# Performance work log

Hardware: AMD Instinct MI355X
Metric: run time of the kernel (lower is better)

The kernel has to match this reference:

```python
import jax, jax.numpy as jnp
import numpy as np

B, S, F = 256, 512, 26
H, M, C = 512, 256, 20  # rnn_hidden, mlp_hidden, num_classes


def setup_inputs() -> dict:
    key = jax.random.key(0)
    ks = jax.random.split(key, 9)
    s_ih = 1.0 / np.sqrt(H)
    return {
        "x": jax.random.normal(ks[0], (B, S, F), dtype=jnp.float32),
        "w_ih": jax.random.uniform(ks[1], (4 * H, F), jnp.float32, -s_ih, s_ih),
        "w_hh": jax.random.uniform(ks[2], (4 * H, H), jnp.float32, -s_ih, s_ih),
        "b_ih": jax.random.uniform(ks[3], (4 * H,), jnp.float32, -s_ih, s_ih),
        "b_hh": jax.random.uniform(ks[4], (4 * H,), jnp.float32, -s_ih, s_ih),
        "w1": jax.random.uniform(ks[5], (M, H), jnp.float32, -s_ih, s_ih),
        "b1": jax.random.uniform(ks[6], (M,), jnp.float32, -s_ih, s_ih),
        "w2": jax.random.uniform(ks[7], (C, M), jnp.float32, -1.0 / np.sqrt(M), 1.0 / np.sqrt(M)),
        "b2": jax.random.uniform(ks[8], (C,), jnp.float32, -1.0 / np.sqrt(M), 1.0 / np.sqrt(M)),
    }


def reference(x, w_ih, w_hh, b_ih, b_hh, w1, b1, w2, b2):
    b, s, _ = x.shape
    h0 = jnp.zeros((b, H), x.dtype)
    c0 = jnp.zeros((b, H), x.dtype)
    bias = b_ih + b_hh

    def step(carry, xt):
        h, c = carry
        # original stores hx.data -> state carried into next step is detached
        h = jax.lax.stop_gradient(h)
        c = jax.lax.stop_gradient(c)
        z = xt @ w_ih.T + h @ w_hh.T + bias  # [b, 4H]
        i, f, g, o = jnp.split(z, 4, axis=-1)  # PyTorch gate order i,f,g,o
        c2 = jax.nn.sigmoid(f) * c + jax.nn.sigmoid(i) * jnp.tanh(g)
        h2 = jax.nn.sigmoid(o) * jnp.tanh(c2)
        return (h2, c2), h2

    _, hs = jax.lax.scan(step, (h0, c0), jnp.transpose(x, (1, 0, 2)))  # hs: [s, b, H]
    hs = jnp.transpose(hs, (1, 0, 2))  # [b, s, H]
    hidden = jax.nn.relu(jnp.einsum("bsh,mh->bsm", hs, w1) + b1)
    logits = jnp.einsum("bsm,cm->bsc", hidden, w2) + b2
    return jax.nn.log_softmax(logits, axis=-1)
```

## Files before the change

kernel.cpp:

```cpp
#include <hip/hip_runtime.h>

#define S_LEN 512
#define HID   512
#define FEAT  26
#define NCLS  20
#define DRING 16

typedef short bf16x8 __attribute__((ext_vector_type(8)));
typedef float f32x4  __attribute__((ext_vector_type(4)));

__device__ __forceinline__ unsigned short f2bf(float f) {
    unsigned u = __builtin_bit_cast(unsigned, f);
    unsigned r = (u + 0x7FFFu + ((u >> 16) & 1u)) >> 16;
    return (unsigned short)r;
}
__device__ __forceinline__ float sigm(float x) { return 1.f / (1.f + __expf(-x)); }
__device__ __forceinline__ float tanh_f(float x) {
    float xc = fminf(fmaxf(x, -15.f), 15.f);
    float t = __expf(-2.f * xc);
    return (1.f - t) / (1.f + t);
}

__device__ __forceinline__ void load4_coherent(const unsigned short* p,
                                               uint4& a0, uint4& a1, uint4& a2, uint4& a3) {
    asm volatile(
        "global_load_dwordx4 %0, %4, off sc0 sc1\n\t"
        "global_load_dwordx4 %1, %5, off sc0 sc1\n\t"
        "global_load_dwordx4 %2, %6, off sc0 sc1\n\t"
        "global_load_dwordx4 %3, %7, off sc0 sc1\n\t"
        "s_waitcnt vmcnt(0)"
        : "=&v"(a0), "=&v"(a1), "=&v"(a2), "=&v"(a3)
        : "v"(p), "v"(p + 8), "v"(p + 16), "v"(p + 24)
        : "memory");
}
__device__ __forceinline__ void store_coherent(unsigned short* p, unsigned d) {
    asm volatile(
        "global_store_dword %0, %1, off sc0 sc1\n\t"
        "s_waitcnt vmcnt(0)"
        :: "v"(p), "v"(d) : "memory");
}
__device__ __forceinline__ void store_coherent_x2(unsigned short* p, unsigned long long d) {
    asm volatile(
        "global_store_dwordx2 %0, %1, off sc0 sc1\n\t"
        "s_waitcnt vmcnt(0)"
        :: "v"(p), "v"(d) : "memory");
}
__device__ __forceinline__ void store_u32_nowait(unsigned* p, unsigned d) {
    asm volatile("global_store_dword %0, %1, off sc0 sc1" :: "v"(p), "v"(d) : "memory");
}
__device__ __forceinline__ unsigned load_u32_coherent(const unsigned* p) {
    unsigned v;
    asm volatile("global_load_dword %0, %1, off sc0 sc1\n\ts_waitcnt vmcnt(0)"
                 : "=v"(v) : "v"(p) : "memory");
    return v;
}

__global__ void prep_kernel(const float* __restrict__ w1, const float* __restrict__ w2,
                            unsigned short* __restrict__ w1b, unsigned short* __restrict__ w2b,
                            unsigned* __restrict__ syncw, int nclear) {
    int i = blockIdx.x * 256 + threadIdx.x;
    if (i < nclear) syncw[i] = 0u;
    if (i < 256 * 512) w1b[i] = f2bf(w1[i]);
    if (i < NCLS * 256) w2b[i] = f2bf(w2[i]);
}

__global__ __launch_bounds__(256, 1) void lstm_big_kernel(
    const float* __restrict__ x,
    const float* __restrict__ w_ih,
    const float* __restrict__ w_hh,
    const float* __restrict__ b_ih,
    const float* __restrict__ b_hh,
    const unsigned short* __restrict__ w1b,
    const float* __restrict__ b1,
    const unsigned short* __restrict__ w2b,
    const float* __restrict__ b2,
    float* __restrict__ out,
    unsigned short* __restrict__ hs,
    unsigned* __restrict__ flags)
{
    const int tid  = threadIdx.x;
    const int wave = tid >> 6;
    const int lane = tid & 63;
    const int quad = lane >> 4;
    const int l16  = lane & 15;
    const int wg   = blockIdx.x;

    __shared__ __align__(16) unsigned short At[16 * 552];
    __shared__ float zb[16 * 260];
    __shared__ __align__(16) unsigned short hid[16 * 264];
    __shared__ float lg[16 * 24];
    __shared__ unsigned rdy;
    if (tid == 0) rdy = 0u;
    __syncthreads();

    if (wg < 128) {
        const int clust = wg >> 3;
        const int wic   = wg & 7;
        const int B0    = clust * 16;
        const int U0    = wic * 64;

        bf16x8 bB[4][17];
#pragma unroll
        for (int tl = 0; tl < 4; ++tl) {
            const int row = wave * 512 + U0 + tl * 16 + l16;
            const float* wrow = w_hh + (size_t)row * HID;
#pragma unroll
            for (int kk = 0; kk < 16; ++kk) {
                const float* p = wrow + kk * 32 + quad * 8;
                bf16x8 v;
#pragma unroll
                for (int j = 0; j < 8; ++j) v[j] = (short)f2bf(p[j]);
                bB[tl][kk] = v;
            }
            const float* irow = w_ih + (size_t)row * FEAT;
            bf16x8 v;
#pragma unroll
            for (int j = 0; j < 8; ++j) {
                int ftr = quad * 8 + j;
                v[j] = (ftr < FEAT) ? (short)f2bf(irow[ftr]) : (short)0;
            }
            bB[tl][16] = v;
        }

        const int gb = tid >> 4;
        const int gu = tid & 15;
        float bias[4][4];
#pragma unroll
        for (int uu = 0; uu < 4; ++uu)
#pragma unroll
            for (int g = 0; g < 4; ++g) {
                int r = g * 512 + U0 + 4 * gu + uu;
                bias[uu][g] = b_ih[r] + b_hh[r];
            }
        float cst[4] = {0.f, 0.f, 0.f, 0.f};

        const int sm = tid >> 4;
        const int sc = tid & 15;
        unsigned short* hsc = hs + (size_t)clust * S_LEN * 16 * HID;
        unsigned* myflag = flags + (clust * 8 + wic) * 16;
        const unsigned* peer = flags + (clust * 8 + (lane & 7)) * 16;

        for (int t = 0; t < S_LEN; ++t) {
            {
                unsigned pk = 0u;
                if (sc <= 12) {
                    float2 xv = *(const float2*)(x + ((size_t)(B0 + sm) * S_LEN + t) * FEAT + sc * 2);
                    pk = (unsigned)f2bf(xv.x) | ((unsigned)f2bf(xv.y) << 16);
                }
                *(unsigned*)(At + sm * 552 + 512 + sc * 2) = pk;
            }
            if (t > 0) {
                if (wave == 0) {
                    for (;;) {
                        unsigned v = load_u32_coherent(peer);
                        if (__ballot(v >= (unsigned)t) == ~0ull) break;
                        __builtin_amdgcn_s_sleep(1);
                    }
                    if (lane == 0)
                        __hip_atomic_store(&rdy, (unsigned)t, __ATOMIC_RELAXED,
                                           __HIP_MEMORY_SCOPE_WORKGROUP);
                } else {
                    while (__hip_atomic_load(&rdy, __ATOMIC_RELAXED,
                                             __HIP_MEMORY_SCOPE_WORKGROUP) < (unsigned)t)
                        __builtin_amdgcn_s_sleep(1);
                }
                const unsigned short* src =
                    hsc + ((size_t)(t - 1) * 16 + sm) * HID + sc * 32;
                unsigned short* dst = At + sm * 552 + sc * 32;
                uint4 a0, a1, a2, a3;
                load4_coherent(src, a0, a1, a2, a3);
                *(uint4*)(dst)      = a0;
                *(uint4*)(dst + 8)  = a1;
                *(uint4*)(dst + 16) = a2;
                *(uint4*)(dst + 24) = a3;
            }
            __syncthreads();

            f32x4 acc[4];
#pragma unroll
            for (int tl = 0; tl < 4; ++tl) acc[tl] = (f32x4){0.f, 0.f, 0.f, 0.f};
            const unsigned short* arow = At + l16 * 552 + quad * 8;
            if (t > 0) {
#pragma unroll
                for (int kk = 0; kk < 17; ++kk) {
                    bf16x8 a = __builtin_bit_cast(bf16x8, *(const uint4*)(arow + kk * 32));
#pragma unroll
                    for (int tl = 0; tl < 4; ++tl)
                        acc[tl] = __builtin_amdgcn_mfma_f32_16x16x32_bf16(a, bB[tl][kk], acc[tl], 0, 0, 0);
                }
            } else {
                bf16x8 a = __builtin_bit_cast(bf16x8, *(const uint4*)(arow + 16 * 32));
#pragma unroll
                for (int tl = 0; tl < 4; ++tl)
                    acc[tl] = __builtin_amdgcn_mfma_f32_16x16x32_bf16(a, bB[tl][16], acc[tl], 0, 0, 0);
            }
#pragma unroll
            for (int tl = 0; tl < 4; ++tl)
#pragma unroll
                for (int r = 0; r < 4; ++r)
                    zb[(quad * 4 + r) * 260 + wave * 64 + tl * 16 + l16] = acc[tl][r];
            __syncthreads();

            {
                const float* zrow = zb + gb * 260;
                unsigned short hv[4];
#pragma unroll
                for (int uu = 0; uu < 4; ++uu) {
                    int u = 4 * gu + uu;
                    float zi = zrow[u]       + bias[uu][0];
                    float zf = zrow[64 + u]  + bias[uu][1];
                    float zg = zrow[128 + u] + bias[uu][2];
                    float zo = zrow[192 + u] + bias[uu][3];
                    float cn = sigm(zf) * cst[uu] + sigm(zi) * tanh_f(zg);
                    cst[uu] = cn;
                    hv[uu] = f2bf(sigm(zo) * tanh_f(cn));
                }
                unsigned long long d = (unsigned long long)hv[0]
                                     | ((unsigned long long)hv[1] << 16)
                                     | ((unsigned long long)hv[2] << 32)
                                     | ((unsigned long long)hv[3] << 48);
                unsigned short* hp = hsc + ((size_t)t * 16 + gb) * HID + U0 + 4 * gu;
                store_coherent_x2(hp, d);
            }
            __syncthreads();
            if (tid == 0) store_u32_nowait(myflag, (unsigned)(t + 1));
        }
    } else {
        const int mwg  = wg - 128;
        const int mc   = mwg >> 3;
        const int m    = mwg & 7;
        const int B0   = mc * 16;
        const unsigned* peer = flags + (mc * 8 + (lane & 7)) * 16;
        const unsigned short* hsc = hs + (size_t)mc * S_LEN * 16 * HID;
        const int sm = tid >> 4;
        const int sc = tid & 15;

        for (int t = m; t < S_LEN; t += 8) {
            if (wave == 0) {
                for (;;) {
                    unsigned v = load_u32_coherent(peer);
                    if (__ballot(v >= (unsigned)(t + 1)) == ~0ull) break;
                    __builtin_amdgcn_s_sleep(8);
                }
                if (lane == 0)
                    __hip_atomic_store(&rdy, (unsigned)(t + 1), __ATOMIC_RELAXED,
                                       __HIP_MEMORY_SCOPE_WORKGROUP);
            } else {
                while (__hip_atomic_load(&rdy, __ATOMIC_RELAXED,
                                         __HIP_MEMORY_SCOPE_WORKGROUP) < (unsigned)(t + 1))
                    __builtin_amdgcn_s_sleep(8);
            }
            {
                const unsigned short* src = hsc + ((size_t)t * 16 + sm) * HID + sc * 32;
                unsigned short* dst = At + sm * 552 + sc * 32;
                uint4 a0, a1, a2, a3;
                load4_coherent(src, a0, a1, a2, a3);
                *(uint4*)(dst)      = a0;
                *(uint4*)(dst + 8)  = a1;
                *(uint4*)(dst + 16) = a2;
                *(uint4*)(dst + 24) = a3;
            }
            __syncthreads();

            f32x4 a1[4];
#pragma unroll
            for (int nt = 0; nt < 4; ++nt) a1[nt] = (f32x4){0.f, 0.f, 0.f, 0.f};
#pragma unroll
            for (int kk = 0; kk < 16; ++kk) {
                bf16x8 a = __builtin_bit_cast(
                    bf16x8, *(const uint4*)(At + l16 * 552 + kk * 32 + quad * 8));
#pragma unroll
                for (int nt = 0; nt < 4; ++nt) {
                    int n = wave * 64 + nt * 16 + l16;
                    bf16x8 b = __builtin_bit_cast(
                        bf16x8, *(const uint4*)(w1b + (size_t)n * 512 + kk * 32 + quad * 8));
                    a1[nt] = __builtin_amdgcn_mfma_f32_16x16x32_bf16(a, b, a1[nt], 0, 0, 0);
                }
            }
#pragma unroll
            for (int nt = 0; nt < 4; ++nt) {
                int n = wave * 64 + nt * 16 + l16;
                float bv = b1[n];
#pragma unroll
                for (int r = 0; r < 4; ++r)
                    hid[(quad * 4 + r) * 264 + n] = f2bf(fmaxf(a1[nt][r] + bv, 0.f));
            }
            __syncthreads();
            if (wave == 0) {
                f32x4 a2[2];
                a2[0] = (f32x4){0.f, 0.f, 0.f, 0.f};
                a2[1] = (f32x4){0.f, 0.f, 0.f, 0.f};
#pragma unroll
                for (int kk = 0; kk < 8; ++kk) {
                    bf16x8 a = __builtin_bit_cast(
                        bf16x8, *(const uint4*)(hid + l16 * 264 + kk * 32 + quad * 8));
#pragma unroll
                    for (int nt = 0; nt < 2; ++nt) {
                        int n = nt * 16 + l16;
                        bf16x8 b;
                        if (n < NCLS) {
                            b = __builtin_bit_cast(
                                bf16x8, *(const uint4*)(w2b + (size_t)n * 256 + kk * 32 + quad * 8));
                        } else {
                            uint4 z; z.x = z.y = z.z = z.w = 0u;
                            b = __builtin_bit_cast(bf16x8, z);
                        }
                        a2[nt] = __builtin_amdgcn_mfma_f32_16x16x32_bf16(a, b, a2[nt], 0, 0, 0);
                    }
                }
#pragma unroll
                for (int nt = 0; nt < 2; ++nt) {
                    int n = nt * 16 + l16;
                    if (n < NCLS) {
                        float bv = b2[n];
#pragma unroll
                        for (int r = 0; r < 4; ++r)
                            lg[(quad * 4 + r) * 24 + n] = a2[nt][r] + bv;
                    }
                }
            }
            __syncthreads();
            if (tid < 16) {
                float v[NCLS];
                float mx = -3.4e38f;
#pragma unroll
                for (int c = 0; c < NCLS; ++c) { v[c] = lg[tid * 24 + c]; mx = fmaxf(mx, v[c]); }
                float s = 0.f;
#pragma unroll
                for (int c = 0; c < NCLS; ++c) s += __expf(v[c] - mx);
                float lse = mx + __logf(s);
                float* orow = out + ((size_t)(B0 + tid) * S_LEN + t) * NCLS;
#pragma unroll
                for (int c = 0; c < NCLS; ++c) orow[c] = v[c] - lse;
            }
            __syncthreads();
        }
    }
}

__global__ __launch_bounds__(256, 2) void lstm_fused_kernel(
    const float* __restrict__ x, const float* __restrict__ w_ih,
    const float* __restrict__ w_hh, const float* __restrict__ b_ih,
    const float* __restrict__ b_hh, const unsigned short* __restrict__ w1b,
    const float* __restrict__ b1, const unsigned short* __restrict__ w2b,
    const float* __restrict__ b2, float* __restrict__ out,
    unsigned short* __restrict__ hb, unsigned* __restrict__ flags,
    unsigned* __restrict__ done)
{
    const int tid  = threadIdx.x;
    const int wave = tid >> 6;
    const int lane = tid & 63;
    const int quad = lane >> 4;
    const int l16  = lane & 15;
    const int wg   = blockIdx.x;

    __shared__ __align__(16) unsigned short At[16 * 552];
    __shared__ float zb[16 * 132];
    __shared__ __align__(16) unsigned short hid[16 * 264];
    __shared__ float lg[16 * 24];
    __shared__ unsigned rdy;
    if (tid == 0) rdy = 0u;
    __syncthreads();

    if (wg < 256) {
        const int clust = (wg & 7) * 2 + (wg >= 128 ? 1 : 0);
        const int wic   = (wg >> 3) & 15;
        const int B0    = clust * 16;
        const int U0    = wic * 32;

        bf16x8 bB[2][17];
#pragma unroll
        for (int tl = 0; tl < 2; ++tl) {
            const int row = wave * 512 + U0 + tl * 16 + l16;
            const float* wrow = w_hh + (size_t)row * HID;
#pragma unroll
            for (int kk = 0; kk < 16; ++kk) {
                const float* p = wrow + kk * 32 + quad * 8;
                bf16x8 v;
#pragma unroll
                for (int j = 0; j < 8; ++j) v[j] = (short)f2bf(p[j]);
                bB[tl][kk] = v;
            }
            const float* irow = w_ih + (size_t)row * FEAT;
            bf16x8 v;
#pragma unroll
            for (int j = 0; j < 8; ++j) {
                int ftr = quad * 8 + j;
                v[j] = (ftr < FEAT) ? (short)f2bf(irow[ftr]) : (short)0;
            }
            bB[tl][16] = v;
        }

        const int gb = tid >> 4;
        const int gu = tid & 15;
        float bias[2][4];
#pragma unroll
        for (int uu = 0; uu < 2; ++uu)
#pragma unroll
            for (int g = 0; g < 4; ++g) {
                int r = g * 512 + U0 + 2 * gu + uu;
                bias[uu][g] = b_ih[r] + b_hh[r];
            }
        float cst[2] = {0.f, 0.f};

        const int sm = tid >> 4;
        const int sc = tid & 15;
        unsigned short* hbc = hb + (size_t)clust * DRING * 16 * HID;
        unsigned* myflag = flags + (clust * 16 + wic) * 16;
        const unsigned* peer = flags + (clust * 16 + (lane & 15)) * 16;

        for (int t = 0; t < S_LEN; ++t) {
            {
                unsigned pk = 0u;
                if (sc <= 12) {
                    float2 xv = *(const float2*)(x + ((size_t)(B0 + sm) * S_LEN + t) * FEAT + sc * 2);
                    pk = (unsigned)f2bf(xv.x) | ((unsigned)f2bf(xv.y) << 16);
                }
                *(unsigned*)(At + sm * 552 + 512 + sc * 2) = pk;
            }
            if (t > 0) {
                if (wave == 0) {
                    if (t >= DRING && lane == 0) {
                        const unsigned* dn = done + (clust * 8 + (t & 7)) * 16;
                        while (load_u32_coherent(dn) < (unsigned)(t - (DRING - 1)))
                            __builtin_amdgcn_s_sleep(8);
                    }
                    for (;;) {
                        unsigned v = load_u32_coherent(peer);
                        if (__ballot(v >= (unsigned)t) == ~0ull) break;
                        __builtin_amdgcn_s_sleep(1);
                    }
                    if (lane == 0)
                        __hip_atomic_store(&rdy, (unsigned)t, __ATOMIC_RELAXED,
                                           __HIP_MEMORY_SCOPE_WORKGROUP);
                } else {
                    while (__hip_atomic_load(&rdy, __ATOMIC_RELAXED,
                                             __HIP_MEMORY_SCOPE_WORKGROUP) < (unsigned)t)
                        __builtin_amdgcn_s_sleep(1);
                }
                const unsigned short* src =
                    hbc + ((t - 1) & (DRING - 1)) * 16 * HID + sm * HID + sc * 32;
                unsigned short* dst = At + sm * 552 + sc * 32;
                uint4 a0, a1, a2, a3;
                load4_coherent(src, a0, a1, a2, a3);
                *(uint4*)(dst)      = a0;
                *(uint4*)(dst + 8)  = a1;
                *(uint4*)(dst + 16) = a2;
                *(uint4*)(dst + 24) = a3;
            }
            __syncthreads();

            f32x4 acc0 = {0.f, 0.f, 0.f, 0.f};
            f32x4 acc1 = {0.f, 0.f, 0.f, 0.f};
            const unsigned short* arow = At + l16 * 552 + quad * 8;
            if (t > 0) {
#pragma unroll
                for (int kk = 0; kk < 17; ++kk) {
                    bf16x8 a = __builtin_bit_cast(bf16x8, *(const uint4*)(arow + kk * 32));
                    acc0 = __builtin_amdgcn_mfma_f32_16x16x32_bf16(a, bB[0][kk], acc0, 0, 0, 0);
                    acc1 = __builtin_amdgcn_mfma_f32_16x16x32_bf16(a, bB[1][kk], acc1, 0, 0, 0);
                }
            } else {
                bf16x8 a = __builtin_bit_cast(bf16x8, *(const uint4*)(arow + 16 * 32));
                acc0 = __builtin_amdgcn_mfma_f32_16x16x32_bf16(a, bB[0][16], acc0, 0, 0, 0);
                acc1 = __builtin_amdgcn_mfma_f32_16x16x32_bf16(a, bB[1][16], acc1, 0, 0, 0);
            }
#pragma unroll
            for (int r = 0; r < 4; ++r) {
                zb[(quad * 4 + r) * 132 + wave * 32 + l16]      = acc0[r];
                zb[(quad * 4 + r) * 132 + wave * 32 + 16 + l16] = acc1[r];
            }
            __syncthreads();

            {
                const float* zrow = zb + gb * 132;
                unsigned short hv2[2];
#pragma unroll
                for (int uu = 0; uu < 2; ++uu) {
                    int u = 2 * gu + uu;
                    float zi = zrow[u]      + bias[uu][0];
                    float zf = zrow[32 + u] + bias[uu][1];
                    float zg = zrow[64 + u] + bias[uu][2];
                    float zo = zrow[96 + u] + bias[uu][3];
                    float cn = sigm(zf) * cst[uu] + sigm(zi) * tanh_f(zg);
                    cst[uu] = cn;
                    hv2[uu] = f2bf(sigm(zo) * tanh_f(cn));
                }
                unsigned short* hp =
                    hbc + (t & (DRING - 1)) * 16 * HID + gb * HID + U0 + 2 * gu;
                store_coherent(hp, (unsigned)hv2[0] | ((unsigned)hv2[1] << 16));
            }
            __syncthreads();
            if (tid == 0) store_u32_nowait(myflag, (unsigned)(t + 1));
        }
    } else {
        const int mwg  = wg - 256;
        const int mc   = mwg >> 3;
        const int m    = mwg & 7;
        const int B0   = mc * 16;
        unsigned* mydone = done + (mc * 8 + m) * 16;
        const unsigned* peer = flags + (mc * 16 + (lane & 15)) * 16;
        const unsigned short* hbc = hb + (size_t)mc * DRING * 16 * HID;
        const int sm = tid >> 4;
        const int sc = tid & 15;

        for (int t = m; t < S_LEN; t += 8) {
            if (wave == 0) {
                for (;;) {
                    unsigned v = load_u32_coherent(peer);
                    if (__ballot(v >= (unsigned)(t + 1)) == ~0ull) break;
                    __builtin_amdgcn_s_sleep(8);
                }
                if (lane == 0)
                    __hip_atomic_store(&rdy, (unsigned)(t + 1), __ATOMIC_RELAXED,
                                       __HIP_MEMORY_SCOPE_WORKGROUP);
            } else {
                while (__hip_atomic_load(&rdy, __ATOMIC_RELAXED,
                                         __HIP_MEMORY_SCOPE_WORKGROUP) < (unsigned)(t + 1))
                    __builtin_amdgcn_s_sleep(8);
            }
            {
                const unsigned short* src =
                    hbc + (t & (DRING - 1)) * 16 * HID + sm * HID + sc * 32;
                unsigned short* dst = At + sm * 552 + sc * 32;
                uint4 a0, a1, a2, a3;
                load4_coherent(src, a0, a1, a2, a3);
                *(uint4*)(dst)      = a0;
                *(uint4*)(dst + 8)  = a1;
                *(uint4*)(dst + 16) = a2;
                *(uint4*)(dst + 24) = a3;
            }
            __syncthreads();
            if (tid == 0) store_u32_nowait(mydone, (unsigned)(t + 1));

            f32x4 a1[4];
#pragma unroll
            for (int nt = 0; nt < 4; ++nt) a1[nt] = (f32x4){0.f, 0.f, 0.f, 0.f};
#pragma unroll
            for (int kk = 0; kk < 16; ++kk) {
                bf16x8 a = __builtin_bit_cast(
                    bf16x8, *(const uint4*)(At + l16 * 552 + kk * 32 + quad * 8));
#pragma unroll
                for (int nt = 0; nt < 4; ++nt) {
                    int n = wave * 64 + nt * 16 + l16;
                    bf16x8 b = __builtin_bit_cast(
                        bf16x8, *(const uint4*)(w1b + (size_t)n * 512 + kk * 32 + quad * 8));
                    a1[nt] = __builtin_amdgcn_mfma_f32_16x16x32_bf16(a, b, a1[nt], 0, 0, 0);
                }
            }
#pragma unroll
            for (int nt = 0; nt < 4; ++nt) {
                int n = wave * 64 + nt * 16 + l16;
                float bv = b1[n];
#pragma unroll
                for (int r = 0; r < 4; ++r)
                    hid[(quad * 4 + r) * 264 + n] = f2bf(fmaxf(a1[nt][r] + bv, 0.f));
            }
            __syncthreads();
            if (wave == 0) {
                f32x4 a2[2];
                a2[0] = (f32x4){0.f, 0.f, 0.f, 0.f};
                a2[1] = (f32x4){0.f, 0.f, 0.f, 0.f};
#pragma unroll
                for (int kk = 0; kk < 8; ++kk) {
                    bf16x8 a = __builtin_bit_cast(
                        bf16x8, *(const uint4*)(hid + l16 * 264 + kk * 32 + quad * 8));
#pragma unroll
                    for (int nt = 0; nt < 2; ++nt) {
                        int n = nt * 16 + l16;
                        bf16x8 b;
                        if (n < NCLS) {
                            b = __builtin_bit_cast(
                                bf16x8, *(const uint4*)(w2b + (size_t)n * 256 + kk * 32 + quad * 8));
                        } else {
                            uint4 z; z.x = z.y = z.z = z.w = 0u;
                            b = __builtin_bit_cast(bf16x8, z);
                        }
                        a2[nt] = __builtin_amdgcn_mfma_f32_16x16x32_bf16(a, b, a2[nt], 0, 0, 0);
                    }
                }
#pragma unroll
                for (int nt = 0; nt < 2; ++nt) {
                    int n = nt * 16 + l16;
                    if (n < NCLS) {
                        float bv = b2[n];
#pragma unroll
                        for (int r = 0; r < 4; ++r)
                            lg[(quad * 4 + r) * 24 + n] = a2[nt][r] + bv;
                    }
                }
            }
            __syncthreads();
            if (tid < 16) {
                float v[NCLS];
                float mx = -3.4e38f;
#pragma unroll
                for (int c = 0; c < NCLS; ++c) { v[c] = lg[tid * 24 + c]; mx = fmaxf(mx, v[c]); }
                float s = 0.f;
#pragma unroll
                for (int c = 0; c < NCLS; ++c) s += __expf(v[c] - mx);
                float lse = mx + __logf(s);
                float* orow = out + ((size_t)(B0 + tid) * S_LEN + t) * NCLS;
#pragma unroll
                for (int c = 0; c < NCLS; ++c) orow[c] = v[c] - lse;
            }
            __syncthreads();
        }
    }
}

extern "C" void kernel_launch(void* const* d_in, const int* in_sizes, int n_in,
                              void* d_out, int out_size, void* d_ws, size_t ws_size,
                              hipStream_t stream) {
    const float* x    = (const float*)d_in[0];
    const float* w_ih = (const float*)d_in[1];
    const float* w_hh = (const float*)d_in[2];
    const float* b_ih = (const float*)d_in[3];
    const float* b_hh = (const float*)d_in[4];
    const float* w1   = (const float*)d_in[5];
    const float* b1   = (const float*)d_in[6];
    const float* w2   = (const float*)d_in[7];
    const float* b2   = (const float*)d_in[8];
    char* ws = (char*)d_ws;

    const size_t HS_BYTES = (size_t)16 * S_LEN * 16 * HID * 2;
    const size_t NEED_BIG = HS_BYTES + 8192 + 262144 + 10240;

    if (ws_size >= NEED_BIG) {
        unsigned short* hsb   = (unsigned short*)ws;
        unsigned*       flags = (unsigned*)(ws + HS_BYTES);
        unsigned short* w1b   = (unsigned short*)(ws + HS_BYTES + 8192);
        unsigned short* w2b   = (unsigned short*)(ws + HS_BYTES + 8192 + 262144);
        prep_kernel<<<512, 256, 0, stream>>>(w1, w2, w1b, w2b, flags, 2048);
        lstm_big_kernel<<<256, 256, 0, stream>>>(x, w_ih, w_hh, b_ih, b_hh,
                                                 w1b, b1, w2b, b2,
                                                 (float*)d_out, hsb, flags);
    } else {
        unsigned short* hb    = (unsigned short*)ws;
        unsigned*       flags = (unsigned*)(ws + 4194304);
        unsigned*       done  = (unsigned*)(ws + 4194304 + 16384);
        unsigned short* w1b   = (unsigned short*)(ws + 4194304 + 16384 + 8192);
        unsigned short* w2b   = (unsigned short*)(ws + 4194304 + 16384 + 8192 + 262144);
        prep_kernel<<<512, 256, 0, stream>>>(w1, w2, w1b, w2b, flags, 6144);
        lstm_fused_kernel<<<384, 256, 0, stream>>>(x, w_ih, w_hh, b_ih, b_hh,
                                                   w1b, b1, w2b, b2,
                                                   (float*)d_out, hb, flags, done);
    }
}
```

Before: 2.103 ms.

## Restructure LSTM step so each wave owns all four gates of its units

Weight rows are remapped so each wave holds the i,f,g,o gate tiles for the same 16 hidden units, letting the cell update run directly on MFMA accumulators without the zb shared-memory staging and its extra barrier. The A operand (previous h) is loaded straight from global memory into registers per wave instead of staging it through LDS, and x is loaded per lane. Every wave now spins on peer flags itself, replacing the wave-0 poll plus LDS broadcast. This removes two barriers and LDS round trips per timestep, in exchange for 16x redundant global reads of h across waves and scattered 2-byte stores.

```diff
diff --git a/kernel.cpp b/kernel.cpp
--- a/kernel.cpp
+++ b/kernel.cpp
@@ -33,15 +33,45 @@
         : "v"(p), "v"(p + 8), "v"(p + 16), "v"(p + 24)
         : "memory");
 }
+__device__ __forceinline__ void loadA16_coherent(const unsigned short* p, uint4* a) {
+    asm volatile(
+        "global_load_dwordx4 %0, %16, off sc0 sc1\n\t"
+        "global_load_dwordx4 %1, %16, off offset:64 sc0 sc1\n\t"
+        "global_load_dwordx4 %2, %16, off offset:128 sc0 sc1\n\t"
+        "global_load_dwordx4 %3, %16, off offset:192 sc0 sc1\n\t"
+        "global_load_dwordx4 %4, %16, off offset:256 sc0 sc1\n\t"
+        "global_load_dwordx4 %5, %16, off offset:320 sc0 sc1\n\t"
+        "global_load_dwordx4 %6, %16, off offset:384 sc0 sc1\n\t"
+        "global_load_dwordx4 %7, %16, off offset:448 sc0 sc1\n\t"
+        "global_load_dwordx4 %8, %16, off offset:512 sc0 sc1\n\t"
+        "global_load_dwordx4 %9, %16, off offset:576 sc0 sc1\n\t"
+        "global_load_dwordx4 %10, %16, off offset:640 sc0 sc1\n\t"
+        "global_load_dwordx4 %11, %16, off offset:704 sc0 sc1\n\t"
+        "global_load_dwordx4 %12, %16, off offset:768 sc0 sc1\n\t"
+        "global_load_dwordx4 %13, %16, off offset:832 sc0 sc1\n\t"
+        "global_load_dwordx4 %14, %16, off offset:896 sc0 sc1\n\t"
+        "global_load_dwordx4 %15, %16, off offset:960 sc0 sc1\n\t"
+        "s_waitcnt vmcnt(0)"
+        : "=&v"(a[0]), "=&v"(a[1]), "=&v"(a[2]), "=&v"(a[3]),
+          "=&v"(a[4]), "=&v"(a[5]), "=&v"(a[6]), "=&v"(a[7]),
+          "=&v"(a[8]), "=&v"(a[9]), "=&v"(a[10]), "=&v"(a[11]),
+          "=&v"(a[12]), "=&v"(a[13]), "=&v"(a[14]), "=&v"(a[15])
+        : "v"(p) : "memory");
+}
+__device__ __forceinline__ void storeH4_coherent(unsigned short* p,
+                                                 unsigned h0, unsigned h1,
+                                                 unsigned h2, unsigned h3) {
+    asm volatile(
+        "global_store_short %0, %1, off sc0 sc1\n\t"
+        "global_store_short %0, %2, off offset:1024 sc0 sc1\n\t"
+        "global_store_short %0, %3, off offset:2048 sc0 sc1\n\t"
+        "global_store_short %0, %4, off offset:3072 sc0 sc1\n\t"
+        "s_waitcnt vmcnt(0)"
+        :: "v"(p), "v"(h0), "v"(h1), "v"(h2), "v"(h3) : "memory");
+}
 __device__ __forceinline__ void store_coherent(unsigned short* p, unsigned d) {
     asm volatile(
         "global_store_dword %0, %1, off sc0 sc1\n\t"
-        "s_waitcnt vmcnt(0)"
-        :: "v"(p), "v"(d) : "memory");
-}
-__device__ __forceinline__ void store_coherent_x2(unsigned short* p, unsigned long long d) {
-    asm volatile(
-        "global_store_dwordx2 %0, %1, off sc0 sc1\n\t"
         "s_waitcnt vmcnt(0)"
         :: "v"(p), "v"(d) : "memory");
 }
@@ -86,7 +116,6 @@
     const int wg   = blockIdx.x;
 
     __shared__ __align__(16) unsigned short At[16 * 552];
-    __shared__ float zb[16 * 260];
     __shared__ __align__(16) unsigned short hid[16 * 264];
     __shared__ float lg[16 * 24];
     __shared__ unsigned rdy;
@@ -98,11 +127,12 @@
         const int wic   = wg & 7;
         const int B0    = clust * 16;
         const int U0    = wic * 64;
+        const int u     = U0 + wave * 16 + l16;
 
         bf16x8 bB[4][17];
 #pragma unroll
-        for (int tl = 0; tl < 4; ++tl) {
-            const int row = wave * 512 + U0 + tl * 16 + l16;
+        for (int g = 0; g < 4; ++g) {
+            const int row = g * 512 + u;
             const float* wrow = w_hh + (size_t)row * HID;
 #pragma unroll
             for (int kk = 0; kk < 16; ++kk) {
@@ -110,7 +140,7 @@
                 bf16x8 v;
 #pragma unroll
                 for (int j = 0; j < 8; ++j) v[j] = (short)f2bf(p[j]);
-                bB[tl][kk] = v;
+                bB[g][kk] = v;
             }
             const float* irow = w_ih + (size_t)row * FEAT;
             bf16x8 v;
@@ -119,109 +149,71 @@
                 int ftr = quad * 8 + j;
                 v[j] = (ftr < FEAT) ? (short)f2bf(irow[ftr]) : (short)0;
             }
-            bB[tl][16] = v;
+            bB[g][16] = v;
         }
-
-        const int gb = tid >> 4;
-        const int gu = tid & 15;
-        float bias[4][4];
-#pragma unroll
-        for (int uu = 0; uu < 4; ++uu)
-#pragma unroll
-            for (int g = 0; g < 4; ++g) {
-                int r = g * 512 + U0 + 4 * gu + uu;
-                bias[uu][g] = b_ih[r] + b_hh[r];
-            }
+        float bias[4];
+#pragma unroll
+        for (int g = 0; g < 4; ++g) bias[g] = b_ih[g * 512 + u] + b_hh[g * 512 + u];
+
         float cst[4] = {0.f, 0.f, 0.f, 0.f};
 
-        const int sm = tid >> 4;
-        const int sc = tid & 15;
         unsigned short* hsc = hs + (size_t)clust * S_LEN * 16 * HID;
         unsigned* myflag = flags + (clust * 8 + wic) * 16;
         const unsigned* peer = flags + (clust * 8 + (lane & 7)) * 16;
+        const float* xbase = x + (size_t)(B0 + l16) * S_LEN * FEAT;
 
         for (int t = 0; t < S_LEN; ++t) {
-            {
-                unsigned pk = 0u;
-                if (sc <= 12) {
-                    float2 xv = *(const float2*)(x + ((size_t)(B0 + sm) * S_LEN + t) * FEAT + sc * 2);
-                    pk = (unsigned)f2bf(xv.x) | ((unsigned)f2bf(xv.y) << 16);
-                }
-                *(unsigned*)(At + sm * 552 + 512 + sc * 2) = pk;
+            float xr[8];
+#pragma unroll
+            for (int j = 0; j < 8; ++j) {
+                int c = quad * 8 + j;
+                xr[j] = (c < FEAT) ? xbase[(size_t)t * FEAT + c] : 0.f;
             }
             if (t > 0) {
-                if (wave == 0) {
-                    for (;;) {
-                        unsigned v = load_u32_coherent(peer);
-                        if (__ballot(v >= (unsigned)t) == ~0ull) break;
-                        __builtin_amdgcn_s_sleep(1);
-                    }
-                    if (lane == 0)
-                        __hip_atomic_store(&rdy, (unsigned)t, __ATOMIC_RELAXED,
-                                           __HIP_MEMORY_SCOPE_WORKGROUP);
-                } else {
-                    while (__hip_atomic_load(&rdy, __ATOMIC_RELAXED,
-                                             __HIP_MEMORY_SCOPE_WORKGROUP) < (unsigned)t)
-                        __builtin_amdgcn_s_sleep(1);
-                }
-                const unsigned short* src =
-                    hsc + ((size_t)(t - 1) * 16 + sm) * HID + sc * 32;
-                unsigned short* dst = At + sm * 552 + sc * 32;
-                uint4 a0, a1, a2, a3;
-                load4_coherent(src, a0, a1, a2, a3);
-                *(uint4*)(dst)      = a0;
-                *(uint4*)(dst + 8)  = a1;
-                *(uint4*)(dst + 16) = a2;
-                *(uint4*)(dst + 24) = a3;
-            }
-            __syncthreads();
+                for (;;) {
+                    unsigned v = load_u32_coherent(peer);
+                    if (__ballot(v >= (unsigned)t) == ~0ull) break;
+                }
+            }
+            bf16x8 ax;
+#pragma unroll
+            for (int j = 0; j < 8; ++j) ax[j] = (short)f2bf(xr[j]);
 
             f32x4 acc[4];
 #pragma unroll
-            for (int tl = 0; tl < 4; ++tl) acc[tl] = (f32x4){0.f, 0.f, 0.f, 0.f};
-            const unsigned short* arow = At + l16 * 552 + quad * 8;
+            for (int g = 0; g < 4; ++g) acc[g] = (f32x4){0.f, 0.f, 0.f, 0.f};
+#pragma unroll
+            for (int g = 0; g < 4; ++g)
+                acc[g] = __builtin_amdgcn_mfma_f32_16x16x32_bf16(ax, bB[g][16], acc[g], 0, 0, 0);
+
             if (t > 0) {
-#pragma unroll
-                for (int kk = 0; kk < 17; ++kk) {
-                    bf16x8 a = __builtin_bit_cast(bf16x8, *(const uint4*)(arow + kk * 32));
-#pragma unroll
-                    for (int tl = 0; tl < 4; ++tl)
-                        acc[tl] = __builtin_amdgcn_mfma_f32_16x16x32_bf16(a, bB[tl][kk], acc[tl], 0, 0, 0);
-                }
-            } else {
-                bf16x8 a = __builtin_bit_cast(bf16x8, *(const uint4*)(arow + 16 * 32));
-#pragma unroll
-                for (int tl = 0; tl < 4; ++tl)
-                    acc[tl] = __builtin_amdgcn_mfma_f32_16x16x32_bf16(a, bB[tl][16], acc[tl], 0, 0, 0);
-            }
-#pragma unroll
-            for (int tl = 0; tl < 4; ++tl)
-#pragma unroll
-                for (int r = 0; r < 4; ++r)
-                    zb[(quad * 4 + r) * 260 + wave * 64 + tl * 16 + l16] = acc[tl][r];
-            __syncthreads();
-
-            {
-                const float* zrow = zb + gb * 260;
-                unsigned short hv[4];
-#pragma unroll
-                for (int uu = 0; uu < 4; ++uu) {
-                    int u = 4 * gu + uu;
-                    float zi = zrow[u]       + bias[uu][0];
-                    float zf = zrow[64 + u]  + bias[uu][1];
-                    float zg = zrow[128 + u] + bias[uu][2];
-                    float zo = zrow[192 + u] + bias[uu][3];
-                    float cn = sigm(zf) * cst[uu] + sigm(zi) * tanh_f(zg);
-                    cst[uu] = cn;
-                    hv[uu] = f2bf(sigm(zo) * tanh_f(cn));
-                }
-                unsigned long long d = (unsigned long long)hv[0]
-                                     | ((unsigned long long)hv[1] << 16)
-                                     | ((unsigned long long)hv[2] << 32)
-                                     | ((unsigned long long)hv[3] << 48);
-                unsigned short* hp = hsc + ((size_t)t * 16 + gb) * HID + U0 + 4 * gu;
-                store_coherent_x2(hp, d);
-            }
+                uint4 a[16];
+                const unsigned short* abase =
+                    hsc + ((size_t)(t - 1) * 16 + l16) * HID + quad * 8;
+                loadA16_coherent(abase, a);
+#pragma unroll
+                for (int kk = 0; kk < 16; ++kk) {
+                    bf16x8 af = __builtin_bit_cast(bf16x8, a[kk]);
+#pragma unroll
+                    for (int g = 0; g < 4; ++g)
+                        acc[g] = __builtin_amdgcn_mfma_f32_16x16x32_bf16(af, bB[g][kk], acc[g], 0, 0, 0);
+                }
+            }
+
+            unsigned hv[4];
+#pragma unroll
+            for (int r = 0; r < 4; ++r) {
+                float zi = acc[0][r] + bias[0];
+                float zf = acc[1][r] + bias[1];
+                float zg = acc[2][r] + bias[2];
+                float zo = acc[3][r] + bias[3];
+                float cn = sigm(zf) * cst[r] + sigm(zi) * tanh_f(zg);
+                cst[r] = cn;
+                hv[r] = (unsigned)f2bf(sigm(zo) * tanh_f(cn));
+            }
+            unsigned short* hp = hsc + ((size_t)t * 16 + quad * 4) * HID + u;
+            storeH4_coherent(hp, hv[0], hv[1], hv[2], hv[3]);
+
             __syncthreads();
             if (tid == 0) store_u32_nowait(myflag, (unsigned)(t + 1));
         }
```

Result: slower. 2.608 ms (+24.0%).
